# Optimization experiments

Hardware: AMD Instinct MI355X
Metric: run time of the kernel (lower is better)

Reference implementation:

```python
import jax, jax.numpy as jnp
import numpy as np

B, T, D, NH, V, L = 2, 1024, 1024, 16, 32000, 4  # L = blocks * layers_per_block
HD = D // NH
FF = 4 * D


def rmsnorm(x, gamma, beta):
    # matches RMSNorm: mean of squares over last dim (tp pmean is identity on 1 device)
    ms = jnp.mean(jnp.square(x), axis=-1, keepdims=True)
    return (x / jnp.sqrt(ms + 1e-6)) * gamma + beta


def setup_inputs() -> dict:
    key = jax.random.key(0)
    ks = jax.random.split(key, 16)
    s = 0.02
    inp = {
        "tokens": jax.random.randint(ks[0], (B, T), 0, V, dtype=jnp.int32),
        "emb_W": jax.random.normal(ks[1], (V, D), jnp.float32) * s,
        "pos_W": jax.random.normal(ks[2], (T, D), jnp.float32) * s,
        "g1": jnp.ones((L, D), jnp.float32),
        "be1": jnp.zeros((L, D), jnp.float32),
        "Wqkv": jax.random.normal(ks[3], (L, D, 3 * D), jnp.float32) * s,
        "bqkv": jnp.zeros((L, 3 * D), jnp.float32),
        "Wo": jax.random.normal(ks[4], (L, D, D), jnp.float32) * s,
        "bo": jnp.zeros((L, D), jnp.float32),
        "g2": jnp.ones((L, D), jnp.float32),
        "be2": jnp.zeros((L, D), jnp.float32),
        "Wf1": jax.random.normal(ks[5], (L, D, FF), jnp.float32) * s,
        "bf1": jnp.zeros((L, FF), jnp.float32),
        "Wf2": jax.random.normal(ks[6], (L, FF, D), jnp.float32) * s,
        "bf2": jnp.zeros((L, D), jnp.float32),
        "gf": jnp.ones((D,), jnp.float32),
        "bef": jnp.zeros((D,), jnp.float32),
    }
    return inp


def _forward(tokens, emb_W, pos_W, g1, be1, Wqkv, bqkv, Wo, bo, g2, be2,
             Wf1, bf1, Wf2, bf2, gf, bef):
    x = emb_W[tokens] + pos_W[jnp.arange(T)]  # [B, T, D]
    causal = jnp.tril(jnp.ones((T, T), dtype=bool))
    scale = HD ** -0.5
    for i in range(L):
        # attention sub-block
        h = rmsnorm(x, g1[i], be1[i])
        qkv = h @ Wqkv[i] + bqkv[i]
        q, k, v = jnp.split(qkv, 3, axis=-1)
        q = q.reshape(B, T, NH, HD).transpose(0, 2, 1, 3)  # B nh T d
        k = k.reshape(B, T, NH, HD).transpose(0, 2, 1, 3)
        v = v.reshape(B, T, NH, HD).transpose(0, 2, 1, 3)
        att = jnp.einsum('bhqd,bhkd->bhqk', q, k) * scale
        att = jnp.where(causal, att, -jnp.inf)
        att = jax.nn.softmax(att, axis=-1)
        o = jnp.einsum('bhqk,bhkd->bhqd', att, v)
        o = o.transpose(0, 2, 1, 3).reshape(B, T, D)
        x = x + (o @ Wo[i] + bo[i])
        # FFN sub-block (selu, dropout off since train=False)
        h = rmsnorm(x, g2[i], be2[i])
        f = jax.nn.selu(h @ Wf1[i] + bf1[i]) @ Wf2[i] + bf2[i]
        x = x + f
    # tied output head: final RMSNorm then embedding.attend
    x = rmsnorm(x, gf, bef)
    logits = jnp.einsum('btd,vd->btv', x, emb_W)
    return logits


def reference(tokens, emb_W, pos_W, g1, be1, Wqkv, bqkv, Wo, bo, g2, be2,
              Wf1, bf1, Wf2, bf2, gf, bef):
    return _forward(tokens, emb_W, pos_W, g1, be1, Wqkv, bqkv, Wo, bo,
                    g2, be2, Wf1, bf1, Wf2, bf2, gf, bef)
```

## Files before the change

### kernel.cpp

```cpp
#include <hip/hip_runtime.h>

typedef unsigned short u16;
typedef __attribute__((ext_vector_type(8))) short bf16x8;
typedef __attribute__((ext_vector_type(4))) float f32x4;

#define DD 1024
#define TT 1024
#define NHH 16
#define VV 32000
#define FFF 4096
#define LL 4
#define MM 2048
#define TD3 3072

__device__ __forceinline__ u16 f2bfu(float f) {
  unsigned int x = __builtin_bit_cast(unsigned int, f);
  return (u16)((x + 0x7FFFu + ((x >> 16) & 1u)) >> 16);
}

__device__ __forceinline__ void gl16(const u16* g, u16* l) {
  __builtin_amdgcn_global_load_lds((const __attribute__((address_space(1))) void*)g,
                                   (__attribute__((address_space(3))) void*)l, 16, 0, 0);
}

template <int N>
__device__ __forceinline__ void vwait() {
  if constexpr (N == 0) asm volatile("s_waitcnt vmcnt(0)" ::: "memory");
  else if constexpr (N == 4) asm volatile("s_waitcnt vmcnt(4)" ::: "memory");
  else asm volatile("s_waitcnt vmcnt(8)" ::: "memory");
}

__global__ void transpose_cvt_k(const float* __restrict__ in, u16* __restrict__ out,
                                int K, int N) {
  const size_t mat = (size_t)K * N;
  in += (size_t)blockIdx.z * mat;
  out += (size_t)blockIdx.z * mat;
  __shared__ float tile[32][65];
  const int n0 = blockIdx.x << 6, k0 = blockIdx.y << 5;
  const int tx = threadIdx.x, ty = threadIdx.y;
#pragma unroll
  for (int i = 0; i < 8; ++i)
    tile[(ty << 3) + i][tx] = in[(size_t)(k0 + (ty << 3) + i) * N + n0 + tx];
  __syncthreads();
  const int tid = (ty << 6) + tx;
  const int n = tid >> 2, oct = (tid & 3) << 3;
  union { u16 s[8]; uint4 u[1]; ulong2 v; } tmp;
#pragma unroll
  for (int j = 0; j < 8; ++j) tmp.s[j] = f2bfu(tile[oct + j][n]);
  *(uint4*)(out + (size_t)(n0 + n) * K + k0 + oct) = tmp.u[0];
}

__global__ void cvt_bf16_k(const float* __restrict__ in, u16* __restrict__ out, long n4) {
  const long i = (long)blockIdx.x * blockDim.x + threadIdx.x;
  if (i >= n4) return;
  const float4 v = ((const float4*)in)[i];
  ushort4 o;
  o.x = f2bfu(v.x); o.y = f2bfu(v.y); o.z = f2bfu(v.z); o.w = f2bfu(v.w);
  ((ushort4*)out)[i] = o;
}

__global__ void embed_k(const int* __restrict__ tok, const float* __restrict__ emb,
                        const float* __restrict__ pos, float* __restrict__ x) {
  const int m = blockIdx.x, tid = threadIdx.x;
  const int t = m & (TT - 1);
  const int id = tok[m];
  const float4 e = ((const float4*)(emb + (size_t)id * DD))[tid];
  const float4 p = ((const float4*)(pos + (size_t)t * DD))[tid];
  float4 r;
  r.x = e.x + p.x; r.y = e.y + p.y; r.z = e.z + p.z; r.w = e.w + p.w;
  ((float4*)(x + (size_t)m * DD))[tid] = r;
}

__global__ void rmsnorm_k(const float* __restrict__ x, const float* __restrict__ g,
                          const float* __restrict__ be, u16* __restrict__ out) {
  const int row = blockIdx.x, tid = threadIdx.x;
  const float4 xv = ((const float4*)(x + (size_t)row * DD))[tid];
  float ss = xv.x * xv.x + xv.y * xv.y + xv.z * xv.z + xv.w * xv.w;
#pragma unroll
  for (int o = 32; o; o >>= 1) ss += __shfl_xor(ss, o);
  __shared__ float sm[4];
  if ((tid & 63) == 0) sm[tid >> 6] = ss;
  __syncthreads();
  const float tot = sm[0] + sm[1] + sm[2] + sm[3];
  const float rs = rsqrtf(tot * (1.f / DD) + 1e-6f);
  const float4 gv = ((const float4*)g)[tid];
  const float4 bv = ((const float4*)be)[tid];
  ushort4 o4;
  o4.x = f2bfu(xv.x * rs * gv.x + bv.x);
  o4.y = f2bfu(xv.y * rs * gv.y + bv.y);
  o4.z = f2bfu(xv.z * rs * gv.z + bv.z);
  o4.w = f2bfu(xv.w * rs * gv.w + bv.w);
  ((ushort4*)(out + (size_t)row * DD))[tid] = o4;
}

template <int NP>
__global__ void addres_rms_k(float* __restrict__ x, const float* __restrict__ pp,
                             const float* __restrict__ bias, const float* __restrict__ g,
                             const float* __restrict__ be, u16* __restrict__ out) {
  const int row = blockIdx.x, tid = threadIdx.x;
  const size_t base = (size_t)row * (DD / 4) + tid;
  float4 s = ((float4*)x)[base];
  const float4 bv = ((const float4*)bias)[tid];
  s.x += bv.x; s.y += bv.y; s.z += bv.z; s.w += bv.w;
#pragma unroll
  for (int p = 0; p < NP; ++p) {
    const float4 pv = ((const float4*)pp)[(size_t)p * (MM * DD / 4) + base];
    s.x += pv.x; s.y += pv.y; s.z += pv.z; s.w += pv.w;
  }
  ((float4*)x)[base] = s;
  float ss = s.x * s.x + s.y * s.y + s.z * s.z + s.w * s.w;
#pragma unroll
  for (int o = 32; o; o >>= 1) ss += __shfl_xor(ss, o);
  __shared__ float sm[4];
  if ((tid & 63) == 0) sm[tid >> 6] = ss;
  __syncthreads();
  const float tot = sm[0] + sm[1] + sm[2] + sm[3];
  const float rs = rsqrtf(tot * (1.f / DD) + 1e-6f);
  const float4 gv = ((const float4*)g)[tid];
  const float4 bev = ((const float4*)be)[tid];
  ushort4 o4;
  o4.x = f2bfu(s.x * rs * gv.x + bev.x);
  o4.y = f2bfu(s.y * rs * gv.y + bev.y);
  o4.z = f2bfu(s.z * rs * gv.z + bev.z);
  o4.w = f2bfu(s.w * rs * gv.w + bev.w);
  ((ushort4*)(out + (size_t)row * DD))[tid] = o4;
}

__global__ void pack_vt_k(const u16* __restrict__ qkv, u16* __restrict__ Vt) {
  const int z = blockIdx.x;
  const int t0 = blockIdx.y << 6;
  const int b = z >> 4, h = z & 15;
  __shared__ u16 tile[64][72];
  const int tid = threadIdx.x;
  for (int c = tid; c < 512; c += 256) {
    const int t = c >> 3, d8 = (c & 7) << 3;
    union { uint4 u; u16 s[8]; } tmp;
    tmp.u = *(const uint4*)(qkv + (long)(b * TT + t0 + t) * TD3 + 2 * DD + h * 64 + d8);
#pragma unroll
    for (int j = 0; j < 8; ++j) tile[d8 + j][t] = tmp.s[j];
  }
  __syncthreads();
  for (int c = tid; c < 512; c += 256) {
    const int d = c >> 3, t8 = (c & 7) << 3;
    *(uint4*)(Vt + ((long)z * 64 + d) * TT + t0 + t8) = *(const uint4*)&tile[d][t8];
  }
}

__global__ __launch_bounds__(256) void flash_k(const u16* __restrict__ qkv,
                                               const u16* __restrict__ Vt,
                                               u16* __restrict__ o) {
  const int z = blockIdx.x;
  const int pair = blockIdx.y;
  const int b = z >> 4, h = z & 15;
  const int tid = threadIdx.x;
  const int lane = tid & 63;
  const int w = tid >> 6;

  __shared__ u16 Qs[64 * 64];
  __shared__ u16 Ks[128 * 64];
  __shared__ u16 Vs[64 * 128];
  __shared__ u16 Ps[64 * 128];

  const u16* qbase = qkv + (size_t)b * TT * TD3;
  const int kcb = (lane >> 4) << 4;

  for (int half = 0; half < 2; ++half) {
    const int qa = half ? (15 - pair) : pair;
    const int q0 = qa << 6;
    const int nkt = (qa >> 1) + 1;

#pragma unroll
    for (int c = 0; c < 2; ++c) {
      const int rbase = c * 32 + w * 8;
      const int row = rbase + (lane >> 3);
      const u16* src = qbase + (long)(q0 + row) * TD3 + h * 64 +
                       ((((lane & 7) << 4) ^ ((row & 7) << 4)) >> 1);
      gl16(src, &Qs[rbase * 64]);
    }

    float m_r[4], l_r[4];
    f32x4 oacc[4];
#pragma unroll
    for (int r = 0; r < 4; ++r) { m_r[r] = -1e30f; l_r[r] = 0.f; }
#pragma unroll
    for (int nd = 0; nd < 4; ++nd) oacc[nd] = (f32x4){0.f, 0.f, 0.f, 0.f};

    for (int kt = 0; kt < nkt; ++kt) {
      const int t0 = kt << 7;
#pragma unroll
      for (int c = 0; c < 4; ++c) {
        const int rbase = c * 32 + w * 8;
        const int row = rbase + (lane >> 3);
        const u16* src = qbase + (long)(t0 + row) * TD3 + DD + h * 64 +
                         ((((lane & 7) << 4) ^ ((row & 7) << 4)) >> 1);
        gl16(src, &Ks[rbase * 64]);
      }
#pragma unroll
      for (int c = 0; c < 4; ++c) {
        const int rbase = c * 16 + w * 4;
        const int d = rbase + (lane >> 4);
        const u16* src = Vt + ((long)(z * 64 + d)) * TT + t0 +
                         ((((lane & 15) << 4) ^ ((d & 7) << 4)) >> 1);
        gl16(src, &Vs[rbase * 128]);
      }
      __syncthreads();

      f32x4 sacc[8];
#pragma unroll
      for (int ni = 0; ni < 8; ++ni) sacc[ni] = (f32x4){0.f, 0.f, 0.f, 0.f};
      const int qrow = (w << 4) + (lane & 15);
#pragma unroll
      for (int ks = 0; ks < 2; ++ks) {
        const bf16x8 aq = *(const bf16x8*)&Qs[qrow * 64 + (((ks * 64 + kcb) ^ ((qrow & 7) << 4)) >> 1)];
#pragma unroll
        for (int ni = 0; ni < 8; ++ni) {
          const int key = (lane & 15) + (ni << 4);
          const bf16x8 bk = *(const bf16x8*)&Ks[key * 64 + (((ks * 64 + kcb) ^ ((key & 7) << 4)) >> 1)];
          sacc[ni] = __builtin_amdgcn_mfma_f32_16x16x32_bf16(aq, bk, sacc[ni], 0, 0, 0);
        }
      }

      float mx[4] = {-1e30f, -1e30f, -1e30f, -1e30f};
      const bool diag = (kt == nkt - 1);
#pragma unroll
      for (int ni = 0; ni < 8; ++ni)
#pragma unroll
        for (int r = 0; r < 4; ++r) {
          float v = sacc[ni][r] * 0.125f;
          if (diag) {
            const int key = t0 + (lane & 15) + (ni << 4);
            const int qq = q0 + (w << 4) + ((lane >> 4) << 2) + r;
            if (key > qq) v = -1e30f;
          }
          sacc[ni][r] = v;
          mx[r] = fmaxf(mx[r], v);
        }
#pragma unroll
      for (int st = 1; st < 16; st <<= 1)
#pragma unroll
        for (int r = 0; r < 4; ++r) mx[r] = fmaxf(mx[r], __shfl_xor(mx[r], st));
      float sc[4], sum[4];
#pragma unroll
      for (int r = 0; r < 4; ++r) {
        const float mn = fmaxf(m_r[r], mx[r]);
        sc[r] = __expf(m_r[r] - mn);
        m_r[r] = mn;
        sum[r] = 0.f;
      }
#pragma unroll
      for (int ni = 0; ni < 8; ++ni)
#pragma unroll
        for (int r = 0; r < 4; ++r) {
          const float e = __expf(sacc[ni][r] - m_r[r]);
          sum[r] += e;
          const int prow = (w << 4) + ((lane >> 4) << 2) + r;
          const int pcol = (lane & 15) + (ni << 4);
          Ps[prow * 128 + (((pcol << 1) ^ ((prow & 7) << 4)) >> 1)] = f2bfu(e);
        }
#pragma unroll
      for (int st = 1; st < 16; st <<= 1)
#pragma unroll
        for (int r = 0; r < 4; ++r) sum[r] += __shfl_xor(sum[r], st);
#pragma unroll
      for (int r = 0; r < 4; ++r) l_r[r] = l_r[r] * sc[r] + sum[r];
#pragma unroll
      for (int nd = 0; nd < 4; ++nd)
#pragma unroll
        for (int r = 0; r < 4; ++r) oacc[nd][r] *= sc[r];

#pragma unroll
      for (int ks2 = 0; ks2 < 4; ++ks2) {
        const int prow = (w << 4) + (lane & 15);
        const bf16x8 pa = *(const bf16x8*)&Ps[prow * 128 + (((ks2 * 64 + kcb) ^ ((prow & 7) << 4)) >> 1)];
#pragma unroll
        for (int nd = 0; nd < 4; ++nd) {
          const int dd2 = (lane & 15) + (nd << 4);
          const bf16x8 vb = *(const bf16x8*)&Vs[dd2 * 128 + (((ks2 * 64 + kcb) ^ ((dd2 & 7) << 4)) >> 1)];
          oacc[nd] = __builtin_amdgcn_mfma_f32_16x16x32_bf16(pa, vb, oacc[nd], 0, 0, 0);
        }
      }
      __syncthreads();
    }

    float inv[4];
#pragma unroll
    for (int r = 0; r < 4; ++r) inv[r] = 1.f / l_r[r];
#pragma unroll
    for (int nd = 0; nd < 4; ++nd)
#pragma unroll
      for (int r = 0; r < 4; ++r) {
        const int row = q0 + (w << 4) + ((lane >> 4) << 2) + r;
        const int col = (h << 6) + (lane & 15) + (nd << 4);
        o[(long)(b * TT + row) * DD + col] = f2bfu(oacc[nd][r] * inv[r]);
      }
  }
}

enum { EPI_BF16 = 0, EPI_BF16_BIAS = 1, EPI_SELU = 2, EPI_F32 = 3, EPI_RESID = 4 };

template <int EPI>
__global__ __launch_bounds__(256) void gemm_bt(
    const u16* __restrict__ A, long az1, long az2, int lda,
    const u16* __restrict__ Bt, long bz1, long bz2, int ldb,
    void* __restrict__ C, long cz1, long cz2, int ldc,
    const float* __restrict__ bias, int Nvalid, int K) {
  const int z = blockIdx.z;
  A += (long)(z >> 4) * az1 + (long)(z & 15) * az2;
  Bt += (long)(z >> 4) * bz1 + (long)(z & 15) * bz2;
  const long coff = (long)(z >> 4) * cz1 + (long)(z & 15) * cz2;

  __shared__ u16 ldsA[2][128 * 32];
  __shared__ u16 ldsB[2][128 * 32];

  const int tid = threadIdx.x;
  const int lane = tid & 63;
  const int wave = tid >> 6;
  const int wr = wave >> 1, wc = wave & 1;
  const int m0 = blockIdx.x << 7, n0 = blockIdx.y << 7;

  f32x4 acc[4][4];
#pragma unroll
  for (int i = 0; i < 4; ++i)
#pragma unroll
    for (int j = 0; j < 4; ++j) acc[i][j] = (f32x4){0.f, 0.f, 0.f, 0.f};

  auto STAGE = [&](int buf, int kt) {
    const int k0 = kt << 5;
#pragma unroll
    for (int p = 0; p < 2; ++p) {
      const int c = tid + (p << 8);
      const int row = c >> 2, col = (c & 3) << 3;
      gl16(A + (long)(m0 + row) * lda + k0 + col, &ldsA[buf][c << 3]);
      gl16(Bt + (long)(n0 + row) * ldb + k0 + col, &ldsB[buf][c << 3]);
    }
  };

  const int nk = K >> 5;
  STAGE(0, 0);
  __syncthreads();
  int cur = 0;
  for (int kt = 0; kt < nk; ++kt) {
    if (kt + 1 < nk) STAGE(cur ^ 1, kt + 1);
    const int rb = lane & 15;
    const int kc = (lane >> 4) << 3;
    bf16x8 af[4], bfr[4];
#pragma unroll
    for (int mi = 0; mi < 4; ++mi)
      af[mi] = *(const bf16x8*)&ldsA[cur][(((wr << 6) + (mi << 4) + rb) << 5) + kc];
#pragma unroll
    for (int ni = 0; ni < 4; ++ni)
      bfr[ni] = *(const bf16x8*)&ldsB[cur][(((wc << 6) + (ni << 4) + rb) << 5) + kc];
#pragma unroll
    for (int mi = 0; mi < 4; ++mi)
#pragma unroll
      for (int ni = 0; ni < 4; ++ni)
        acc[mi][ni] = __builtin_amdgcn_mfma_f32_16x16x32_bf16(af[mi], bfr[ni], acc[mi][ni], 0, 0, 0);
    __syncthreads();
    cur ^= 1;
  }

  const int row0 = m0 + (wr << 6) + ((lane >> 4) << 2);
  const int col0 = n0 + (wc << 6) + (lane & 15);
#pragma unroll
  for (int ni = 0; ni < 4; ++ni) {
    const int col = col0 + (ni << 4);
    if (col >= Nvalid) continue;
    float bv = 0.f;
    if (EPI == EPI_BF16_BIAS || EPI == EPI_SELU || EPI == EPI_RESID) bv = bias[col];
#pragma unroll
    for (int mi = 0; mi < 4; ++mi) {
#pragma unroll
      for (int r = 0; r < 4; ++r) {
        const int row = row0 + (mi << 4) + r;
        const long idx = coff + (long)row * ldc + col;
        float v = acc[mi][ni][r] + bv;
        if (EPI == EPI_SELU)
          v = v > 0.f ? 1.0507009873554805f * v : 1.7580993408473766f * (__expf(v) - 1.f);
        if (EPI == EPI_BF16 || EPI == EPI_BF16_BIAS || EPI == EPI_SELU)
          ((u16*)C)[idx] = f2bfu(v);
        else if (EPI == EPI_F32)
          ((float*)C)[idx] = v;
        else
          ((float*)C)[idx] += v;
      }
    }
  }
}

template <int EPI>
__global__ __launch_bounds__(256) void gemm_bt3(
    const u16* __restrict__ A, long az1, long az2, int lda,
    const u16* __restrict__ Bt, long bz1, long bz2, int ldb,
    void* __restrict__ C, long cz1, long cz2, int ldc,
    const float* __restrict__ bias, int Nvalid, int K) {
  const int z = blockIdx.z;
  A += (long)(z >> 4) * az1 + (long)(z & 15) * az2;
  Bt += (long)(z >> 4) * bz1 + (long)(z & 15) * bz2;
  const long coff = (long)(z >> 4) * cz1 + (long)(z & 15) * cz2;

  __shared__ u16 ldsA[3][128 * 32];
  __shared__ u16 ldsB[3][128 * 32];

  const int tid = threadIdx.x;
  const int lane = tid & 63;
  const int wave = tid >> 6;
  const int wr = wave >> 1, wc = wave & 1;
  const int m0 = blockIdx.x << 7, n0 = blockIdx.y << 7;

  f32x4 acc[4][4];
#pragma unroll
  for (int i = 0; i < 4; ++i)
#pragma unroll
    for (int j = 0; j < 4; ++j) acc[i][j] = (f32x4){0.f, 0.f, 0.f, 0.f};

  auto STAGE = [&](int buf, int kt) {
    const int k0 = kt << 5;
#pragma unroll
    for (int p = 0; p < 2; ++p) {
      const int c = tid + (p << 8);
      const int row = c >> 2, col = (c & 3) << 3;
      gl16(A + (long)(m0 + row) * lda + k0 + col, &ldsA[buf][c << 3]);
      gl16(Bt + (long)(n0 + row) * ldb + k0 + col, &ldsB[buf][c << 3]);
    }
  };

  const int nk = K >> 5;
  STAGE(0, 0);
  STAGE(1, 1);

  const int rb = lane & 15;
  const int kc = (lane >> 4) << 3;
  int cur = 0, stg = 2;
#pragma unroll 1
  for (int kt = 0; kt < nk; ++kt) {
    if (kt + 1 < nk) vwait<4>();
    else vwait<0>();
    __builtin_amdgcn_s_barrier();
    __builtin_amdgcn_sched_barrier(0);

    bf16x8 af[4], bfr[4];
#pragma unroll
    for (int mi = 0; mi < 4; ++mi)
      af[mi] = *(const bf16x8*)&ldsA[cur][(((wr << 6) + (mi << 4) + rb) << 5) + kc];
#pragma unroll
    for (int ni = 0; ni < 4; ++ni)
      bfr[ni] = *(const bf16x8*)&ldsB[cur][(((wc << 6) + (ni << 4) + rb) << 5) + kc];
    asm volatile("s_waitcnt lgkmcnt(0)" ::: "memory");
    __builtin_amdgcn_sched_barrier(0);
    __builtin_amdgcn_s_barrier();
    __builtin_amdgcn_sched_barrier(0);
    if (kt + 2 < nk) STAGE(stg, kt + 2);
    __builtin_amdgcn_sched_barrier(0);

    __builtin_amdgcn_s_setprio(1);
#pragma unroll
    for (int mi = 0; mi < 4; ++mi)
#pragma unroll
      for (int ni = 0; ni < 4; ++ni)
        acc[mi][ni] = __builtin_amdgcn_mfma_f32_16x16x32_bf16(af[mi], bfr[ni], acc[mi][ni], 0, 0, 0);
    __builtin_amdgcn_s_setprio(0);

    cur = (cur == 2) ? 0 : cur + 1;
    stg = (stg == 2) ? 0 : stg + 1;
  }

  const int row0 = m0 + (wr << 6) + ((lane >> 4) << 2);
  const int col0 = n0 + (wc << 6) + (lane & 15);
#pragma unroll
  for (int ni = 0; ni < 4; ++ni) {
    const int col = col0 + (ni << 4);
    if (col >= Nvalid) continue;
    float bv = 0.f;
    if (EPI == EPI_BF16_BIAS || EPI == EPI_SELU || EPI == EPI_RESID) bv = bias[col];
#pragma unroll
    for (int mi = 0; mi < 4; ++mi) {
#pragma unroll
      for (int r = 0; r < 4; ++r) {
        const int row = row0 + (mi << 4) + r;
        const long idx = coff + (long)row * ldc + col;
        float v = acc[mi][ni][r] + bv;
        if (EPI == EPI_SELU)
          v = v > 0.f ? 1.0507009873554805f * v : 1.7580993408473766f * (__expf(v) - 1.f);
        if (EPI == EPI_BF16 || EPI == EPI_BF16_BIAS || EPI == EPI_SELU)
          ((u16*)C)[idx] = f2bfu(v);
        else if (EPI == EPI_F32)
          ((float*)C)[idx] = v;
        else
          ((float*)C)[idx] += v;
      }
    }
  }
}

template <int EPI, int KDIM>
__global__ __launch_bounds__(512) void gemm256_k(
    const u16* __restrict__ A, int lda,
    const u16* __restrict__ Bt, int ldb,
    void* __restrict__ C, int ldc,
    const float* __restrict__ bias, int mm) {
  extern __shared__ u16 smem[];
  u16* SA = smem;
  u16* SB = smem + 16384;

  const int nwg = gridDim.x;
  const int q = nwg >> 3, r = nwg & 7;
  const int xcd = blockIdx.x & 7, loc = blockIdx.x >> 3;
  const int wg = (xcd < r) ? (xcd * (q + 1) + loc) : (r * (q + 1) + (xcd - r) * q + loc);
  const int m0 = (wg % mm) << 8;
  const int n0 = (wg / mm) << 8;

  const int tid = threadIdx.x;
  const int lane = tid & 63;
  const int w = tid >> 6;
  const int wr = w >> 2, wc = w & 3;
  const int l = lane & 15, kq = lane >> 4;

  f32x4 acc[8][4];
#pragma unroll
  for (int i = 0; i < 8; ++i)
#pragma unroll
    for (int j = 0; j < 4; ++j) acc[i][j] = (f32x4){0.f, 0.f, 0.f, 0.f};

  auto STAGE = [&](int p, int kt) {
    u16* la = SA + (p << 13);
    u16* lb = SB + (p << 13);
    const int k0 = kt << 5;
#pragma unroll
    for (int hh = 0; hh < 2; ++hh) {
      const int c = tid + (hh << 9);
      const int r2 = c >> 3, sp = c & 7;
      const int s = sp ^ (r2 & 7);
      const int row = r2 + ((s >> 2) << 7);
      const int col = k0 + ((s & 3) << 3);
      gl16(A + (size_t)(m0 + row) * lda + col, la + (c << 3));
      gl16(Bt + (size_t)(n0 + row) * ldb + col, lb + (c << 3));
    }
  };

  constexpr int NK = KDIM >> 5;
  STAGE(0, 0);
  STAGE(1, 1);

  int buf = 0;
#pragma unroll 1
  for (int t = 0; t < NK; ++t) {
    if (t + 1 < NK) vwait<4>();
    else vwait<0>();
    __builtin_amdgcn_s_barrier();
    __builtin_amdgcn_sched_barrier(0);

    const u16* a = SA + (buf << 13);
    const u16* b = SB + (buf << 13);
    auto rdA = [&](int mi) -> bf16x8 {
      const int row = (wr << 7) + (mi << 4) + l;
      const int r2 = row & 127;
      const int sp = (((row >> 7) << 2) + kq) ^ (r2 & 7);
      return *(const bf16x8*)&a[(r2 << 6) + (sp << 3)];
    };
    auto rdB = [&](int ni) -> bf16x8 {
      const int row = (wc << 6) + (ni << 4) + l;
      const int r2 = row & 127;
      const int sp = (((row >> 7) << 2) + kq) ^ (r2 & 7);
      return *(const bf16x8*)&b[(r2 << 6) + (sp << 3)];
    };

    bf16x8 af[8], bfr[4];
#pragma unroll
    for (int ni = 0; ni < 4; ++ni) bfr[ni] = rdB(ni);
#pragma unroll
    for (int mi = 0; mi < 8; ++mi) af[mi] = rdA(mi);
    asm volatile("s_waitcnt lgkmcnt(0)" ::: "memory");
    __builtin_amdgcn_sched_barrier(0);
    __builtin_amdgcn_s_barrier();
    __builtin_amdgcn_sched_barrier(0);
    if (t + 2 < NK) STAGE(buf, t + 2);
    __builtin_amdgcn_sched_barrier(0);

    __builtin_amdgcn_s_setprio(1);
#pragma unroll
    for (int mi = 0; mi < 8; ++mi)
#pragma unroll
      for (int ni = 0; ni < 4; ++ni)
        acc[mi][ni] = __builtin_amdgcn_mfma_f32_16x16x32_bf16(af[mi], bfr[ni], acc[mi][ni], 0, 0, 0);
    __builtin_amdgcn_s_setprio(0);
    buf ^= 1;
  }

  const int row0 = m0 + (wr << 7) + ((lane >> 4) << 2);
  const int col0 = n0 + (wc << 6) + (lane & 15);
#pragma unroll
  for (int ni = 0; ni < 4; ++ni) {
    const int col = col0 + (ni << 4);
    float bv = 0.f;
    if (EPI == EPI_BF16_BIAS || EPI == EPI_SELU) bv = bias[col];
#pragma unroll
    for (int mi = 0; mi < 8; ++mi) {
#pragma unroll
      for (int r = 0; r < 4; ++r) {
        const int row = row0 + (mi << 4) + r;
        const long idx = (long)row * ldc + col;
        float v = acc[mi][ni][r] + bv;
        if (EPI == EPI_SELU)
          v = v > 0.f ? 1.0507009873554805f * v : 1.7580993408473766f * (__expf(v) - 1.f);
        if (EPI == EPI_BF16 || EPI == EPI_BF16_BIAS || EPI == EPI_SELU)
          ((u16*)C)[idx] = f2bfu(v);
        else
          ((float*)C)[idx] = v;
      }
    }
  }
}

extern "C" void kernel_launch(void* const* d_in, const int* in_sizes, int n_in,
                              void* d_out, int out_size, void* d_ws, size_t ws_size,
                              hipStream_t stream) {
  const int* tokens = (const int*)d_in[0];
  const float* emb_W = (const float*)d_in[1];
  const float* pos_W = (const float*)d_in[2];
  const float* g1 = (const float*)d_in[3];
  const float* be1 = (const float*)d_in[4];
  const float* Wqkv = (const float*)d_in[5];
  const float* bqkv = (const float*)d_in[6];
  const float* Wo = (const float*)d_in[7];
  const float* bo = (const float*)d_in[8];
  const float* g2 = (const float*)d_in[9];
  const float* be2 = (const float*)d_in[10];
  const float* Wf1 = (const float*)d_in[11];
  const float* bf1 = (const float*)d_in[12];
  const float* Wf2 = (const float*)d_in[13];
  const float* bf2 = (const float*)d_in[14];
  const float* gf = (const float*)d_in[15];
  const float* bef = (const float*)d_in[16];

  char* w = (char*)d_ws;
  auto alloc = [&](size_t bytes) {
    char* p = w;
    w += (bytes + 255) & ~(size_t)255;
    return p;
  };
  u16* WqkvT = (u16*)alloc((size_t)LL * TD3 * DD * 2);
  u16* WoT   = (u16*)alloc((size_t)LL * DD * DD * 2);
  u16* Wf1T  = (u16*)alloc((size_t)LL * FFF * DD * 2);
  u16* Wf2T  = (u16*)alloc((size_t)LL * DD * FFF * 2);
  u16* embB  = (u16*)alloc((size_t)VV * DD * 2);
  float* x   = (float*)alloc((size_t)MM * DD * 4);
  u16* h     = (u16*)alloc((size_t)MM * DD * 2);
  u16* qkv   = (u16*)alloc((size_t)MM * TD3 * 2);
  u16* Vt    = (u16*)alloc((size_t)32 * 64 * TT * 2);
  u16* o     = (u16*)alloc((size_t)MM * DD * 2);
  u16* h1    = (u16*)alloc((size_t)MM * FFF * 2);
  float* pp  = (float*)alloc((size_t)4 * MM * DD * 4);

  bool big =
      hipFuncSetAttribute((const void*)&gemm256_k<EPI_F32, 1024>,
                          hipFuncAttributeMaxDynamicSharedMemorySize, 65536) == hipSuccess;

  dim3 tb2(64, 4);
  transpose_cvt_k<<<dim3(TD3 / 64, DD / 32, LL), tb2, 0, stream>>>(Wqkv, WqkvT, DD, TD3);
  transpose_cvt_k<<<dim3(DD / 64, DD / 32, LL), tb2, 0, stream>>>(Wo, WoT, DD, DD);
  transpose_cvt_k<<<dim3(FFF / 64, DD / 32, LL), tb2, 0, stream>>>(Wf1, Wf1T, DD, FFF);
  transpose_cvt_k<<<dim3(DD / 64, FFF / 32, LL), tb2, 0, stream>>>(Wf2, Wf2T, FFF, DD);
  cvt_bf16_k<<<(VV * DD / 4) / 256, 256, 0, stream>>>(emb_W, embB, (long)VV * DD / 4);
  embed_k<<<MM, 256, 0, stream>>>(tokens, emb_W, pos_W, x);
  rmsnorm_k<<<MM, 256, 0, stream>>>(x, g1, be1, h);

  for (int i = 0; i < LL; ++i) {
    gemm_bt3<EPI_BF16_BIAS><<<dim3(16, 24, 1), 256, 0, stream>>>(
        h, 0, 0, DD, WqkvT + (size_t)i * TD3 * DD, 0, 0, DD,
        qkv, 0, 0, TD3, bqkv + i * TD3, TD3, DD);
    pack_vt_k<<<dim3(32, 16), 256, 0, stream>>>(qkv, Vt);
    flash_k<<<dim3(32, 8), 256, 0, stream>>>(qkv, Vt, o);
    gemm_bt3<EPI_F32><<<dim3(16, 8, 2), 256, 0, stream>>>(
        o, 0, 512, DD, WoT + (size_t)i * DD * DD, 0, 512, DD,
        pp, 0, (long)MM * DD, DD, nullptr, DD, 512);
    addres_rms_k<2><<<MM, 256, 0, stream>>>(x, pp, bo + i * DD, g2 + i * DD, be2 + i * DD, h);
    gemm_bt3<EPI_SELU><<<dim3(16, 32, 1), 256, 0, stream>>>(
        h, 0, 0, DD, Wf1T + (size_t)i * FFF * DD, 0, 0, DD,
        h1, 0, 0, FFF, bf1 + i * FFF, FFF, DD);
    gemm_bt3<EPI_F32><<<dim3(16, 8, 4), 256, 0, stream>>>(
        h1, 0, 1024, FFF, Wf2T + (size_t)i * DD * FFF, 0, 1024, FFF,
        pp, 0, (long)MM * DD, DD, nullptr, DD, 1024);
    const bool last = (i == LL - 1);
    addres_rms_k<4><<<MM, 256, 0, stream>>>(
        x, pp, bf2 + i * DD,
        last ? gf : g1 + (i + 1) * DD, last ? bef : be1 + (i + 1) * DD, h);
  }

  if (big) {
    gemm256_k<EPI_F32, 1024><<<1000, 512, 65536, stream>>>(
        h, DD, embB, DD, (float*)d_out, VV, nullptr, 8);
  } else {
    gemm_bt<EPI_F32><<<dim3(16, 250, 1), 256, 0, stream>>>(
        h, 0, 0, DD, embB, 0, 0, DD,
        (float*)d_out, 0, 0, VV, nullptr, VV, DD);
  }
}
```

Before: 960.7 us.

## Rework logits GEMM into 4-phase pipeline with K=64 tiles and split-half staging

Rewrites the 256x256 output-head GEMM to use K=64 tiles stored as separate 128-row half-buffers (128KB LDS), interleaving LDS fragment reads, global-to-LDS prefetches and MFMA bursts across four phases per iteration. A is prefetched one tile ahead and B two halves ahead, spread across the phases to overlap load latency with compute. This roughly halves barrier-bounded iterations per K, at the cost of more barriers per iteration and doubled LDS use. The specialised kernel also drops the generic epilogue template and writes fp32 directly.

```diff
diff --git a/kernel.cpp b/kernel.cpp
--- a/kernel.cpp
+++ b/kernel.cpp
@@ -26,8 +26,7 @@
 template <int N>
 __device__ __forceinline__ void vwait() {
   if constexpr (N == 0) asm volatile("s_waitcnt vmcnt(0)" ::: "memory");
-  else if constexpr (N == 4) asm volatile("s_waitcnt vmcnt(4)" ::: "memory");
-  else asm volatile("s_waitcnt vmcnt(8)" ::: "memory");
+  else asm volatile("s_waitcnt vmcnt(4)" ::: "memory");
 }
 
 __global__ void transpose_cvt_k(const float* __restrict__ in, u16* __restrict__ out,
@@ -44,7 +43,7 @@
   __syncthreads();
   const int tid = (ty << 6) + tx;
   const int n = tid >> 2, oct = (tid & 3) << 3;
-  union { u16 s[8]; uint4 u[1]; ulong2 v; } tmp;
+  union { u16 s[8]; uint4 u[1]; } tmp;
 #pragma unroll
   for (int j = 0; j < 8; ++j) tmp.s[j] = f2bfu(tile[oct + j][n]);
   *(uint4*)(out + (size_t)(n0 + n) * K + k0 + oct) = tmp.u[0];
@@ -492,15 +491,12 @@
   }
 }
 
-template <int EPI, int KDIM>
-__global__ __launch_bounds__(512) void gemm256_k(
+template <int KDIM>
+__global__ __launch_bounds__(512) void gemm256p_k(
     const u16* __restrict__ A, int lda,
     const u16* __restrict__ Bt, int ldb,
-    void* __restrict__ C, int ldc,
-    const float* __restrict__ bias, int mm) {
+    float* __restrict__ C, int ldc, int mm) {
   extern __shared__ u16 smem[];
-  u16* SA = smem;
-  u16* SB = smem + 16384;
 
   const int nwg = gridDim.x;
   const int q = nwg >> 3, r = nwg & 7;
@@ -521,91 +517,112 @@
 #pragma unroll
     for (int j = 0; j < 4; ++j) acc[i][j] = (f32x4){0.f, 0.f, 0.f, 0.f};
 
-  auto STAGE = [&](int p, int kt) {
-    u16* la = SA + (p << 13);
-    u16* lb = SB + (p << 13);
-    const int k0 = kt << 5;
-#pragma unroll
-    for (int hh = 0; hh < 2; ++hh) {
-      const int c = tid + (hh << 9);
-      const int r2 = c >> 3, sp = c & 7;
-      const int s = sp ^ (r2 & 7);
-      const int row = r2 + ((s >> 2) << 7);
-      const int col = k0 + ((s & 3) << 3);
-      gl16(A + (size_t)(m0 + row) * lda + col, la + (c << 3));
-      gl16(Bt + (size_t)(n0 + row) * ldb + col, lb + (c << 3));
+  auto STAGEH = [&](const u16* M, int ld, int base0, int tau, int isB, int h) {
+    u16* dst = smem + (((((tau & 1) << 2) | (isB << 1) | h)) << 13);
+    const int k0 = tau << 6;
+#pragma unroll
+    for (int cc = 0; cc < 2; ++cc) {
+      const int c = tid + (cc << 9);
+      const int row = c >> 3;
+      const int s = (c & 7) ^ (row & 7);
+      gl16(M + (size_t)(base0 + (h << 7) + row) * ld + k0 + (s << 3), dst + (c << 3));
     }
   };
 
-  constexpr int NK = KDIM >> 5;
-  STAGE(0, 0);
-  STAGE(1, 1);
-
-  int buf = 0;
+  auto RD_A = [&](int d, int mi, int kk) -> bf16x8 {
+    const int row = (mi << 4) + l;
+    const u16* p = smem + (((d << 2) | wr) << 13);
+    const int s = ((kk << 2) + kq) ^ (row & 7);
+    return *(const bf16x8*)&p[(row << 6) + (s << 3)];
+  };
+  auto RD_B = [&](int d, int ni, int kk) -> bf16x8 {
+    const int row = ((wc & 1) << 6) + (ni << 4) + l;
+    const u16* p = smem + (((d << 2) | 2 | (wc >> 1)) << 13);
+    const int s = ((kk << 2) + kq) ^ (row & 7);
+    return *(const bf16x8*)&p[(row << 6) + (s << 3)];
+  };
+
+  constexpr int NT = KDIM >> 6;
+
+  STAGEH(Bt, ldb, n0, 0, 1, 0); STAGEH(Bt, ldb, n0, 0, 1, 1);
+  STAGEH(A,  lda, m0, 0, 0, 0); STAGEH(A,  lda, m0, 0, 0, 1);
+  STAGEH(Bt, ldb, n0, 1, 1, 0); STAGEH(Bt, ldb, n0, 1, 1, 1);
+  vwait<4>();
+  __builtin_amdgcn_s_barrier();
+  __builtin_amdgcn_sched_barrier(0);
+
+#define PHASE_MFMA(Q)                                                                   \
+  asm volatile("s_waitcnt lgkmcnt(0)" ::: "memory");                                    \
+  __builtin_amdgcn_sched_barrier(0);                                                    \
+  __builtin_amdgcn_s_setprio(1);                                                        \
+  _Pragma("unroll")                                                                     \
+  for (int kk = 0; kk < 2; ++kk)                                                        \
+    _Pragma("unroll")                                                                   \
+    for (int dm = 0; dm < 2; ++dm)                                                      \
+      _Pragma("unroll")                                                                 \
+      for (int ni = 0; ni < 4; ++ni)                                                    \
+        acc[2 * (Q) + dm][ni] = __builtin_amdgcn_mfma_f32_16x16x32_bf16(                \
+            af[dm][kk], bfr[ni][kk], acc[2 * (Q) + dm][ni], 0, 0, 0);                   \
+  __builtin_amdgcn_s_setprio(0);                                                        \
+  __builtin_amdgcn_sched_barrier(0);
+
 #pragma unroll 1
-  for (int t = 0; t < NK; ++t) {
-    if (t + 1 < NK) vwait<4>();
+  for (int t = 0; t < NT; ++t) {
+    const int d = t & 1;
+    bf16x8 bfr[4][2], af[2][2];
+
+#pragma unroll
+    for (int ni = 0; ni < 4; ++ni) {
+      bfr[ni][0] = RD_B(d, ni, 0);
+      bfr[ni][1] = RD_B(d, ni, 1);
+    }
+    af[0][0] = RD_A(d, 0, 0); af[0][1] = RD_A(d, 0, 1);
+    af[1][0] = RD_A(d, 1, 0); af[1][1] = RD_A(d, 1, 1);
+    if (t + 1 < NT) { STAGEH(A, lda, m0, t + 1, 0, 0); STAGEH(A, lda, m0, t + 1, 0, 1); }
+    __builtin_amdgcn_sched_barrier(0);
+    __builtin_amdgcn_s_barrier();
+    PHASE_MFMA(0)
+    __builtin_amdgcn_s_barrier();
+
+    af[0][0] = RD_A(d, 2, 0); af[0][1] = RD_A(d, 2, 1);
+    af[1][0] = RD_A(d, 3, 0); af[1][1] = RD_A(d, 3, 1);
+    if (t + 2 < NT) STAGEH(Bt, ldb, n0, t + 2, 1, 0);
+    __builtin_amdgcn_sched_barrier(0);
+    __builtin_amdgcn_s_barrier();
+    PHASE_MFMA(1)
+    __builtin_amdgcn_s_barrier();
+
+    af[0][0] = RD_A(d, 4, 0); af[0][1] = RD_A(d, 4, 1);
+    af[1][0] = RD_A(d, 5, 0); af[1][1] = RD_A(d, 5, 1);
+    if (t + 2 < NT) STAGEH(Bt, ldb, n0, t + 2, 1, 1);
+    __builtin_amdgcn_sched_barrier(0);
+    __builtin_amdgcn_s_barrier();
+    PHASE_MFMA(2)
+    __builtin_amdgcn_s_barrier();
+
+    af[0][0] = RD_A(d, 6, 0); af[0][1] = RD_A(d, 6, 1);
+    af[1][0] = RD_A(d, 7, 0); af[1][1] = RD_A(d, 7, 1);
+    __builtin_amdgcn_sched_barrier(0);
+    __builtin_amdgcn_s_barrier();
+    PHASE_MFMA(3)
+    if (t + 2 < NT) vwait<4>();
     else vwait<0>();
-    __builtin_amdgcn_s_barrier();
-    __builtin_amdgcn_sched_barrier(0);
-
-    const u16* a = SA + (buf << 13);
-    const u16* b = SB + (buf << 13);
-    auto rdA = [&](int mi) -> bf16x8 {
-      const int row = (wr << 7) + (mi << 4) + l;
-      const int r2 = row & 127;
-      const int sp = (((row >> 7) << 2) + kq) ^ (r2 & 7);
-      return *(const bf16x8*)&a[(r2 << 6) + (sp << 3)];
-    };
-    auto rdB = [&](int ni) -> bf16x8 {
-      const int row = (wc << 6) + (ni << 4) + l;
-      const int r2 = row & 127;
-      const int sp = (((row >> 7) << 2) + kq) ^ (r2 & 7);
-      return *(const bf16x8*)&b[(r2 << 6) + (sp << 3)];
-    };
-
-    bf16x8 af[8], bfr[4];
-#pragma unroll
-    for (int ni = 0; ni < 4; ++ni) bfr[ni] = rdB(ni);
-#pragma unroll
-    for (int mi = 0; mi < 8; ++mi) af[mi] = rdA(mi);
-    asm volatile("s_waitcnt lgkmcnt(0)" ::: "memory");
-    __builtin_amdgcn_sched_barrier(0);
-    __builtin_amdgcn_s_barrier();
-    __builtin_amdgcn_sched_barrier(0);
-    if (t + 2 < NK) STAGE(buf, t + 2);
-    __builtin_amdgcn_sched_barrier(0);
-
-    __builtin_amdgcn_s_setprio(1);
-#pragma unroll
-    for (int mi = 0; mi < 8; ++mi)
-#pragma unroll
-      for (int ni = 0; ni < 4; ++ni)
-        acc[mi][ni] = __builtin_amdgcn_mfma_f32_16x16x32_bf16(af[mi], bfr[ni], acc[mi][ni], 0, 0, 0);
-    __builtin_amdgcn_s_setprio(0);
-    buf ^= 1;
-  }
-
-  const int row0 = m0 + (wr << 7) + ((lane >> 4) << 2);
-  const int col0 = n0 + (wc << 6) + (lane & 15);
+    __builtin_amdgcn_sched_barrier(0);
+    __builtin_amdgcn_s_barrier();
+  }
+#undef PHASE_MFMA
+
+  const int row0 = m0 + (wr << 7) + (kq << 2);
+  const int col0 = n0 + (wc << 6) + l;
 #pragma unroll
   for (int ni = 0; ni < 4; ++ni) {
     const int col = col0 + (ni << 4);
-    float bv = 0.f;
-    if (EPI == EPI_BF16_BIAS || EPI == EPI_SELU) bv = bias[col];
 #pragma unroll
     for (int mi = 0; mi < 8; ++mi) {
 #pragma unroll
       for (int r = 0; r < 4; ++r) {
         const int row = row0 + (mi << 4) + r;
-        const long idx = (long)row * ldc + col;
-        float v = acc[mi][ni][r] + bv;
-        if (EPI == EPI_SELU)
-          v = v > 0.f ? 1.0507009873554805f * v : 1.7580993408473766f * (__expf(v) - 1.f);
-        if (EPI == EPI_BF16 || EPI == EPI_BF16_BIAS || EPI == EPI_SELU)
-          ((u16*)C)[idx] = f2bfu(v);
-        else
-          ((float*)C)[idx] = v;
+        C[(size_t)row * ldc + col] = acc[mi][ni][r];
       }
     }
   }
@@ -652,8 +669,8 @@
   float* pp  = (float*)alloc((size_t)4 * MM * DD * 4);
 
   bool big =
-      hipFuncSetAttribute((const void*)&gemm256_k<EPI_F32, 1024>,
-                          hipFuncAttributeMaxDynamicSharedMemorySize, 65536) == hipSuccess;
+      hipFuncSetAttribute((const void*)&gemm256p_k<1024>,
+                          hipFuncAttributeMaxDynamicSharedMemorySize, 131072) == hipSuccess;
 
   dim3 tb2(64, 4);
   transpose_cvt_k<<<dim3(TD3 / 64, DD / 32, LL), tb2, 0, stream>>>(Wqkv, WqkvT, DD, TD3);
@@ -687,8 +704,8 @@
   }
 
   if (big) {
-    gemm256_k<EPI_F32, 1024><<<1000, 512, 65536, stream>>>(
-        h, DD, embB, DD, (float*)d_out, VV, nullptr, 8);
+    gemm256p_k<1024><<<1000, 512, 131072, stream>>>(
+        h, DD, embB, DD, (float*)d_out, VV, 8);
   } else {
     gemm_bt<EPI_F32><<<dim3(16, 250, 1), 256, 0, stream>>>(
         h, 0, 0, DD, embB, 0, 0, DD,
```

New measurement: 945.8 us. About the same (-1.6%).

## Replace 256x256 LM-head GEMM with 128x256 triple-buffered kernel at two blocks per CU

Applied to the files above, without the earlier changes.

The output-head GEMM changes from a 512-thread 256x256 tile kernel with double buffering to a 256-thread 128x256 tile kernel with three LDS stages, declared with two workgroups per CU. The aim is more occupancy and deeper prefetch, so load latency is hidden better during the vocabulary projection. The LDS XOR swizzle is dropped in favour of a plain row layout. That may bring bank conflicts on the fragment reads, and the simplified XCD remap assumes the grid is divisible by 8.

```diff
diff --git a/kernel.cpp b/kernel.cpp
--- a/kernel.cpp
+++ b/kernel.cpp
@@ -27,7 +27,7 @@
 __device__ __forceinline__ void vwait() {
   if constexpr (N == 0) asm volatile("s_waitcnt vmcnt(0)" ::: "memory");
   else if constexpr (N == 4) asm volatile("s_waitcnt vmcnt(4)" ::: "memory");
-  else asm volatile("s_waitcnt vmcnt(8)" ::: "memory");
+  else asm volatile("s_waitcnt vmcnt(6)" ::: "memory");
 }
 
 __global__ void transpose_cvt_k(const float* __restrict__ in, u16* __restrict__ out,
@@ -44,7 +44,7 @@
   __syncthreads();
   const int tid = (ty << 6) + tx;
   const int n = tid >> 2, oct = (tid & 3) << 3;
-  union { u16 s[8]; uint4 u[1]; ulong2 v; } tmp;
+  union { u16 s[8]; uint4 u[1]; } tmp;
 #pragma unroll
   for (int j = 0; j < 8; ++j) tmp.s[j] = f2bfu(tile[oct + j][n]);
   *(uint4*)(out + (size_t)(n0 + n) * K + k0 + oct) = tmp.u[0];
@@ -492,48 +492,50 @@
   }
 }
 
-template <int EPI, int KDIM>
-__global__ __launch_bounds__(512) void gemm256_k(
+template <int KDIM>
+__global__ __launch_bounds__(256, 2) void gemm_ht(
     const u16* __restrict__ A, int lda,
     const u16* __restrict__ Bt, int ldb,
-    void* __restrict__ C, int ldc,
-    const float* __restrict__ bias, int mm) {
+    float* __restrict__ C, int ldc, int mm) {
   extern __shared__ u16 smem[];
   u16* SA = smem;
-  u16* SB = smem + 16384;
+  u16* SB = smem + 12288;
 
   const int nwg = gridDim.x;
-  const int q = nwg >> 3, r = nwg & 7;
+  const int q = nwg >> 3;
   const int xcd = blockIdx.x & 7, loc = blockIdx.x >> 3;
-  const int wg = (xcd < r) ? (xcd * (q + 1) + loc) : (r * (q + 1) + (xcd - r) * q + loc);
-  const int m0 = (wg % mm) << 8;
+  const int wg = xcd * q + loc;
+  const int m0 = (wg % mm) << 7;
   const int n0 = (wg / mm) << 8;
 
   const int tid = threadIdx.x;
   const int lane = tid & 63;
   const int w = tid >> 6;
-  const int wr = w >> 2, wc = w & 3;
-  const int l = lane & 15, kq = lane >> 4;
-
-  f32x4 acc[8][4];
-#pragma unroll
-  for (int i = 0; i < 8; ++i)
-#pragma unroll
-    for (int j = 0; j < 4; ++j) acc[i][j] = (f32x4){0.f, 0.f, 0.f, 0.f};
-
-  auto STAGE = [&](int p, int kt) {
-    u16* la = SA + (p << 13);
-    u16* lb = SB + (p << 13);
+  const int wm = w >> 1, wn = w & 1;
+  const int rb = lane & 15;
+  const int kc = (lane >> 4) << 3;
+
+  f32x4 acc[4][8];
+#pragma unroll
+  for (int i = 0; i < 4; ++i)
+#pragma unroll
+    for (int j = 0; j < 8; ++j) acc[i][j] = (f32x4){0.f, 0.f, 0.f, 0.f};
+
+  auto STAGE = [&](int buf, int kt) {
     const int k0 = kt << 5;
-#pragma unroll
-    for (int hh = 0; hh < 2; ++hh) {
-      const int c = tid + (hh << 9);
-      const int r2 = c >> 3, sp = c & 7;
-      const int s = sp ^ (r2 & 7);
-      const int row = r2 + ((s >> 2) << 7);
-      const int col = k0 + ((s & 3) << 3);
-      gl16(A + (size_t)(m0 + row) * lda + col, la + (c << 3));
-      gl16(Bt + (size_t)(n0 + row) * ldb + col, lb + (c << 3));
+    u16* la = SA + buf * 4096;
+    u16* lb = SB + buf * 8192;
+#pragma unroll
+    for (int p = 0; p < 2; ++p) {
+      const int c = tid + (p << 8);
+      const int row = c >> 2, col = (c & 3) << 3;
+      gl16(A + (size_t)(m0 + row) * lda + k0 + col, la + (c << 3));
+    }
+#pragma unroll
+    for (int p = 0; p < 4; ++p) {
+      const int c = tid + (p << 8);
+      const int row = c >> 2, col = (c & 3) << 3;
+      gl16(Bt + (size_t)(n0 + row) * ldb + k0 + col, lb + (c << 3));
     }
   };
 
@@ -541,71 +543,53 @@
   STAGE(0, 0);
   STAGE(1, 1);
 
-  int buf = 0;
+  int cur = 0, stg = 2;
 #pragma unroll 1
-  for (int t = 0; t < NK; ++t) {
-    if (t + 1 < NK) vwait<4>();
+  for (int kt = 0; kt < NK; ++kt) {
+    if (kt + 1 < NK) vwait<6>();
     else vwait<0>();
     __builtin_amdgcn_s_barrier();
     __builtin_amdgcn_sched_barrier(0);
 
-    const u16* a = SA + (buf << 13);
-    const u16* b = SB + (buf << 13);
-    auto rdA = [&](int mi) -> bf16x8 {
-      const int row = (wr << 7) + (mi << 4) + l;
-      const int r2 = row & 127;
-      const int sp = (((row >> 7) << 2) + kq) ^ (r2 & 7);
-      return *(const bf16x8*)&a[(r2 << 6) + (sp << 3)];
-    };
-    auto rdB = [&](int ni) -> bf16x8 {
-      const int row = (wc << 6) + (ni << 4) + l;
-      const int r2 = row & 127;
-      const int sp = (((row >> 7) << 2) + kq) ^ (r2 & 7);
-      return *(const bf16x8*)&b[(r2 << 6) + (sp << 3)];
-    };
-
-    bf16x8 af[8], bfr[4];
-#pragma unroll
-    for (int ni = 0; ni < 4; ++ni) bfr[ni] = rdB(ni);
-#pragma unroll
-    for (int mi = 0; mi < 8; ++mi) af[mi] = rdA(mi);
+    const u16* a = SA + cur * 4096;
+    const u16* b = SB + cur * 8192;
+    bf16x8 af[4], bfr[8];
+#pragma unroll
+    for (int mi = 0; mi < 4; ++mi)
+      af[mi] = *(const bf16x8*)&a[(((wm << 6) + (mi << 4) + rb) << 5) + kc];
+#pragma unroll
+    for (int ni = 0; ni < 8; ++ni)
+      bfr[ni] = *(const bf16x8*)&b[(((wn << 7) + (ni << 4) + rb) << 5) + kc];
     asm volatile("s_waitcnt lgkmcnt(0)" ::: "memory");
     __builtin_amdgcn_sched_barrier(0);
     __builtin_amdgcn_s_barrier();
     __builtin_amdgcn_sched_barrier(0);
-    if (t + 2 < NK) STAGE(buf, t + 2);
+    if (kt + 2 < NK) STAGE(stg, kt + 2);
     __builtin_amdgcn_sched_barrier(0);
 
     __builtin_amdgcn_s_setprio(1);
 #pragma unroll
-    for (int mi = 0; mi < 8; ++mi)
-#pragma unroll
-      for (int ni = 0; ni < 4; ++ni)
+    for (int mi = 0; mi < 4; ++mi)
+#pragma unroll
+      for (int ni = 0; ni < 8; ++ni)
         acc[mi][ni] = __builtin_amdgcn_mfma_f32_16x16x32_bf16(af[mi], bfr[ni], acc[mi][ni], 0, 0, 0);
     __builtin_amdgcn_s_setprio(0);
-    buf ^= 1;
-  }
-
-  const int row0 = m0 + (wr << 7) + ((lane >> 4) << 2);
-  const int col0 = n0 + (wc << 6) + (lane & 15);
-#pragma unroll
-  for (int ni = 0; ni < 4; ++ni) {
+
+    cur = (cur == 2) ? 0 : cur + 1;
+    stg = (stg == 2) ? 0 : stg + 1;
+  }
+
+  const int row0 = m0 + (wm << 6) + ((lane >> 4) << 2);
+  const int col0 = n0 + (wn << 7) + (lane & 15);
+#pragma unroll
+  for (int ni = 0; ni < 8; ++ni) {
     const int col = col0 + (ni << 4);
-    float bv = 0.f;
-    if (EPI == EPI_BF16_BIAS || EPI == EPI_SELU) bv = bias[col];
-#pragma unroll
-    for (int mi = 0; mi < 8; ++mi) {
+#pragma unroll
+    for (int mi = 0; mi < 4; ++mi) {
 #pragma unroll
       for (int r = 0; r < 4; ++r) {
         const int row = row0 + (mi << 4) + r;
-        const long idx = (long)row * ldc + col;
-        float v = acc[mi][ni][r] + bv;
-        if (EPI == EPI_SELU)
-          v = v > 0.f ? 1.0507009873554805f * v : 1.7580993408473766f * (__expf(v) - 1.f);
-        if (EPI == EPI_BF16 || EPI == EPI_BF16_BIAS || EPI == EPI_SELU)
-          ((u16*)C)[idx] = f2bfu(v);
-        else
-          ((float*)C)[idx] = v;
+        C[(size_t)row * ldc + col] = acc[mi][ni][r];
       }
     }
   }
@@ -652,8 +636,8 @@
   float* pp  = (float*)alloc((size_t)4 * MM * DD * 4);
 
   bool big =
-      hipFuncSetAttribute((const void*)&gemm256_k<EPI_F32, 1024>,
-                          hipFuncAttributeMaxDynamicSharedMemorySize, 65536) == hipSuccess;
+      hipFuncSetAttribute((const void*)&gemm_ht<1024>,
+                          hipFuncAttributeMaxDynamicSharedMemorySize, 73728) == hipSuccess;
 
   dim3 tb2(64, 4);
   transpose_cvt_k<<<dim3(TD3 / 64, DD / 32, LL), tb2, 0, stream>>>(Wqkv, WqkvT, DD, TD3);
@@ -687,8 +671,8 @@
   }
 
   if (big) {
-    gemm256_k<EPI_F32, 1024><<<1000, 512, 65536, stream>>>(
-        h, DD, embB, DD, (float*)d_out, VV, nullptr, 8);
+    gemm_ht<1024><<<2000, 256, 73728, stream>>>(
+        h, DD, embB, DD, (float*)d_out, VV, 16);
   } else {
     gemm_bt<EPI_F32><<<dim3(16, 250, 1), 256, 0, stream>>>(
         h, 0, 0, DD, embB, 0, 0, DD,
```

After: 946.2 us. Within noise of the previous version (-1.5%).
